# Kernel tuning notes

Measured on AMD Instinct MI355X. Metric: run time of the kernel, lower is better.

Reference implementation:

```python
import jax, jax.numpy as jnp
import numpy as np

N = 8192
IN_F = 512
OUT_F = 64
ALPHA = 0.2  # LeakyReLU negative slope
NEG_INF = -9e15


def setup_inputs() -> dict:
    key = jax.random.key(0)
    k1, k2, k3, k4 = jax.random.split(key, 4)
    inp = jax.random.normal(k1, (N, IN_F), dtype=jnp.float32)
    adj = jax.random.randint(k2, (N, N), 0, 2, dtype=jnp.int32)
    W = jax.random.normal(k3, (IN_F, OUT_F), dtype=jnp.float32) * (1.414 * (6.0 / (IN_F + OUT_F)) ** 0.5)
    a = jax.random.normal(k4, (2 * OUT_F, 1), dtype=jnp.float32) * (1.414 * (6.0 / (2 * OUT_F + 1)) ** 0.5)
    return {"input": inp, "adj": adj, "W": W, "a": a}


def reference(input, adj, W, a):
    h = input @ W                      # [N, F]
    F_ = h.shape[1]
    # e_ij = leakyrelu(a[:F].h_i + a[F:].h_j)  (equivalent to the concat form)
    f_src = h @ a[:F_, 0]              # [N]
    f_dst = h @ a[F_:, 0]              # [N]
    e = jax.nn.leaky_relu(f_src[:, None] + f_dst[None, :], negative_slope=ALPHA)  # [N, N]
    att = jnp.where(adj > 0, e, jnp.float32(NEG_INF))
    att = jax.nn.softmax(att, axis=1)  # dropout p is inert in eval mode
    h_prime = att @ h                  # [N, F]
    return jax.nn.elu(h_prime)         # concat=True
```

## Files before the change

### kernel.cpp

```cpp
#include <hip/hip_runtime.h>

#define N_NODES 8192
#define IN_F 512
#define OUT_F 64
#define LOG2E 1.4426950408889634f

typedef short bf16x8 __attribute__((ext_vector_type(8)));
typedef float f32x4 __attribute__((ext_vector_type(4)));

__global__ __launch_bounds__(256) void k_gemm(const float* __restrict__ input,
                                              const float* __restrict__ W,
                                              const float* __restrict__ a,
                                              unsigned short* __restrict__ hT,
                                              float* __restrict__ fsrcL,
                                              float* __restrict__ fdstL) {
  const int lane = threadIdx.x & 63;
  const int wv = threadIdx.x >> 6;
  const int r0 = blockIdx.x * 4;
  const int row = r0 + wv;
  const float* inrow = input + (size_t)row * IN_F;
  const int c = lane;
  float acc = 0.f;
  for (int k = 0; k < IN_F; k += 4) {
    float4 x = *(const float4*)(inrow + k);
    acc += x.x * W[(k + 0) * OUT_F + c];
    acc += x.y * W[(k + 1) * OUT_F + c];
    acc += x.z * W[(k + 2) * OUT_F + c];
    acc += x.w * W[(k + 3) * OUT_F + c];
  }
  float vs = acc * a[c];
  float vd = acc * a[OUT_F + c];
#pragma unroll
  for (int off = 32; off > 0; off >>= 1) {
    vs += __shfl_xor(vs, off, 64);
    vd += __shfl_xor(vd, off, 64);
  }
  if (lane == 0) {
    fsrcL[row] = vs * LOG2E;
    fdstL[row] = vd * LOG2E;
  }
  __shared__ float hs[4][64];
  hs[wv][c] = acc;
  __syncthreads();
  if (threadIdx.x < 64) {
    const int cc = threadIdx.x;
    unsigned u0 = __float_as_uint(hs[0][cc]) + 0x8000u;
    unsigned u1 = __float_as_uint(hs[1][cc]) + 0x8000u;
    unsigned u2 = __float_as_uint(hs[2][cc]) + 0x8000u;
    unsigned u3 = __float_as_uint(hs[3][cc]) + 0x8000u;
    uint2 pk;
    pk.x = __builtin_amdgcn_perm(u1, u0, 0x07060302u);
    pk.y = __builtin_amdgcn_perm(u3, u2, 0x07060302u);
    *(uint2*)(hT + (size_t)cc * N_NODES + r0) = pk;
  }
}

__global__ __launch_bounds__(256) void k_max(const float* __restrict__ fdstL,
                                             float* __restrict__ ML) {
  float m = -3.0e38f;
  for (int i = threadIdx.x; i < N_NODES; i += 256) m = fmaxf(m, fdstL[i]);
#pragma unroll
  for (int off = 32; off > 0; off >>= 1) m = fmaxf(m, __shfl_xor(m, off, 64));
  __shared__ float sm[4];
  if ((threadIdx.x & 63) == 0) sm[threadIdx.x >> 6] = m;
  __syncthreads();
  if (threadIdx.x == 0) ML[0] = fmaxf(fmaxf(sm[0], sm[1]), fmaxf(sm[2], sm[3]));
}

__global__ __launch_bounds__(512) void k_attn(const int* __restrict__ adj,
                                              const unsigned short* __restrict__ hT,
                                              const float* __restrict__ fsrcL,
                                              const float* __restrict__ fdstL,
                                              const float* __restrict__ MLp,
                                              float* __restrict__ out) {
  const int lane = threadIdx.x & 63;
  const int wv = threadIdx.x >> 6;
  const int i0 = blockIdx.x * 16;
  const int m = lane & 15;
  const int g = lane >> 4;

  const float MLv = MLp[0];
  const float fs = fsrcL[i0 + m];
  const float xm = fs + MLv;
  const float mL = fmaxf(xm, 0.2f * xm);

  f32x4 acc0{}, acc1{}, acc2{}, acc3{};
  float lpart = 0.f;

  const int* adjrow = adj + (size_t)(i0 + m) * N_NODES;
  const unsigned short* hT0 = hT + (size_t)m * N_NODES;

  const int jbeg = wv * (N_NODES / 8);
  for (int j0 = jbeg; j0 < jbeg + (N_NODES / 8); j0 += 64) {
#pragma unroll
    for (int s = 0; s < 2; s++) {
      const int jb = j0 + s * 32 + g * 8;
      int4 a0 = *(const int4*)(adjrow + jb);
      int4 a1 = *(const int4*)(adjrow + jb + 4);
      float4 d0 = *(const float4*)(fdstL + jb);
      float4 d1 = *(const float4*)(fdstL + jb + 4);
      bf16x8 b0 = *(const bf16x8*)(hT0 + jb);
      bf16x8 b1 = *(const bf16x8*)(hT0 + (size_t)16 * N_NODES + jb);
      bf16x8 b2 = *(const bf16x8*)(hT0 + (size_t)32 * N_NODES + jb);
      bf16x8 b3 = *(const bf16x8*)(hT0 + (size_t)48 * N_NODES + jb);

      const int av[8] = {a0.x, a0.y, a0.z, a0.w, a1.x, a1.y, a1.z, a1.w};
      const float dv[8] = {d0.x, d0.y, d0.z, d0.w, d1.x, d1.y, d1.z, d1.w};
      unsigned u[8];
#pragma unroll
      for (int t = 0; t < 8; t++) {
        float x = fs + dv[t];
        float y = fmaxf(x, 0.2f * x) - mL;
        float p = __builtin_amdgcn_exp2f(y);
        p = av[t] ? p : 0.0f;
        lpart += p;
        u[t] = __float_as_uint(p) + 0x8000u;
      }
      union { unsigned w[4]; bf16x8 v; } pc;
      pc.w[0] = __builtin_amdgcn_perm(u[1], u[0], 0x07060302u);
      pc.w[1] = __builtin_amdgcn_perm(u[3], u[2], 0x07060302u);
      pc.w[2] = __builtin_amdgcn_perm(u[5], u[4], 0x07060302u);
      pc.w[3] = __builtin_amdgcn_perm(u[7], u[6], 0x07060302u);

      acc0 = __builtin_amdgcn_mfma_f32_16x16x32_bf16(pc.v, b0, acc0, 0, 0, 0);
      acc1 = __builtin_amdgcn_mfma_f32_16x16x32_bf16(pc.v, b1, acc1, 0, 0, 0);
      acc2 = __builtin_amdgcn_mfma_f32_16x16x32_bf16(pc.v, b2, acc2, 0, 0, 0);
      acc3 = __builtin_amdgcn_mfma_f32_16x16x32_bf16(pc.v, b3, acc3, 0, 0, 0);
    }
  }

  lpart += __shfl_xor(lpart, 16, 64);
  lpart += __shfl_xor(lpart, 32, 64);

  __shared__ float accbuf[8][16][64];
  __shared__ float lbuf[8][16];
#pragma unroll
  for (int r = 0; r < 4; r++) {
    accbuf[wv][g * 4 + r][0 + m]  = acc0[r];
    accbuf[wv][g * 4 + r][16 + m] = acc1[r];
    accbuf[wv][g * 4 + r][32 + m] = acc2[r];
    accbuf[wv][g * 4 + r][48 + m] = acc3[r];
  }
  if (lane < 16) lbuf[wv][lane] = lpart;
  __syncthreads();

#pragma unroll
  for (int q = 0; q < 2; q++) {
    int idx = q * 512 + threadIdx.x;
    int r = idx >> 6, c = idx & 63;
    float ssum = 0.f, l = 0.f;
#pragma unroll
    for (int w = 0; w < 8; w++) {
      ssum += accbuf[w][r][c];
      l += lbuf[w][r];
    }
    float v = ssum / l;
    out[(size_t)(i0 + r) * OUT_F + c] =
        v > 0.f ? v : __builtin_amdgcn_exp2f(v * LOG2E) - 1.f;
  }
}

extern "C" void kernel_launch(void* const* d_in, const int* in_sizes, int n_in,
                              void* d_out, int out_size, void* d_ws, size_t ws_size,
                              hipStream_t stream) {
  const float* input = (const float*)d_in[0];
  const int* adj = (const int*)d_in[1];
  const float* W = (const float*)d_in[2];
  const float* a = (const float*)d_in[3];
  float* out = (float*)d_out;

  char* ws = (char*)d_ws;
  unsigned short* hT = (unsigned short*)ws;
  float* fsrcL = (float*)(ws + (1u << 20));
  float* fdstL = (float*)(ws + (1u << 20) + 32 * 1024);
  float* ML = (float*)(ws + (1u << 20) + 64 * 1024);

  k_gemm<<<N_NODES / 4, 256, 0, stream>>>(input, W, a, hT, fsrcL, fdstL);
  k_max<<<1, 256, 0, stream>>>(fdstL, ML);
  k_attn<<<N_NODES / 16, 512, 0, stream>>>(adj, hT, fsrcL, fdstL, ML, out);
}
```

Before: 511.4 us.

## Split attention over column blocks with merge kernel, register-tile input GEMM

The attention kernel now splits each 16-row block's neighbour range into four column chunks handled by separate 256-thread blocks. Each block writes partial numerators and denominators, and a new merge kernel sums them and applies the normalisation and ELU. The attention inner loop issues the loads for both 32-column halves up front to get more memory traffic in flight. The input projection kernel computes 8 rows per wave so each W load is reused across those rows, and it writes hT in wider 16-byte packets. The cost is an extra launch and a round trip of the partial sums through global memory.

```diff
diff --git a/kernel.cpp b/kernel.cpp
--- a/kernel.cpp
+++ b/kernel.cpp
@@ -4,6 +4,7 @@
 #define IN_F 512
 #define OUT_F 64
 #define LOG2E 1.4426950408889634f
+#define JSPLIT 4
 
 typedef short bf16x8 __attribute__((ext_vector_type(8)));
 typedef float f32x4 __attribute__((ext_vector_type(4)));
@@ -16,42 +17,53 @@
                                               float* __restrict__ fdstL) {
   const int lane = threadIdx.x & 63;
   const int wv = threadIdx.x >> 6;
-  const int r0 = blockIdx.x * 4;
-  const int row = r0 + wv;
-  const float* inrow = input + (size_t)row * IN_F;
+  const int r0 = blockIdx.x * 32;
+  const int rw = r0 + wv * 8;
   const int c = lane;
-  float acc = 0.f;
+  float acc[8] = {0.f, 0.f, 0.f, 0.f, 0.f, 0.f, 0.f, 0.f};
+  const float* Wc = W + c;
   for (int k = 0; k < IN_F; k += 4) {
-    float4 x = *(const float4*)(inrow + k);
-    acc += x.x * W[(k + 0) * OUT_F + c];
-    acc += x.y * W[(k + 1) * OUT_F + c];
-    acc += x.z * W[(k + 2) * OUT_F + c];
-    acc += x.w * W[(k + 3) * OUT_F + c];
-  }
-  float vs = acc * a[c];
-  float vd = acc * a[OUT_F + c];
-#pragma unroll
-  for (int off = 32; off > 0; off >>= 1) {
-    vs += __shfl_xor(vs, off, 64);
-    vd += __shfl_xor(vd, off, 64);
-  }
-  if (lane == 0) {
-    fsrcL[row] = vs * LOG2E;
-    fdstL[row] = vd * LOG2E;
-  }
-  __shared__ float hs[4][64];
-  hs[wv][c] = acc;
+    float w0 = Wc[(k + 0) * OUT_F];
+    float w1 = Wc[(k + 1) * OUT_F];
+    float w2 = Wc[(k + 2) * OUT_F];
+    float w3 = Wc[(k + 3) * OUT_F];
+#pragma unroll
+    for (int r = 0; r < 8; r++) {
+      float4 x = *(const float4*)(input + (size_t)(rw + r) * IN_F + k);
+      acc[r] += x.x * w0 + x.y * w1 + x.z * w2 + x.w * w3;
+    }
+  }
+#pragma unroll
+  for (int r = 0; r < 8; r++) {
+    float vs = acc[r] * a[c];
+    float vd = acc[r] * a[OUT_F + c];
+#pragma unroll
+    for (int off = 32; off > 0; off >>= 1) {
+      vs += __shfl_xor(vs, off, 64);
+      vd += __shfl_xor(vd, off, 64);
+    }
+    if (lane == 0) {
+      fsrcL[rw + r] = vs * LOG2E;
+      fdstL[rw + r] = vd * LOG2E;
+    }
+  }
+  __shared__ float hs[32][65];
+#pragma unroll
+  for (int r = 0; r < 8; r++) hs[wv * 8 + r][c] = acc[r];
   __syncthreads();
-  if (threadIdx.x < 64) {
-    const int cc = threadIdx.x;
-    unsigned u0 = __float_as_uint(hs[0][cc]) + 0x8000u;
-    unsigned u1 = __float_as_uint(hs[1][cc]) + 0x8000u;
-    unsigned u2 = __float_as_uint(hs[2][cc]) + 0x8000u;
-    unsigned u3 = __float_as_uint(hs[3][cc]) + 0x8000u;
-    uint2 pk;
-    pk.x = __builtin_amdgcn_perm(u1, u0, 0x07060302u);
-    pk.y = __builtin_amdgcn_perm(u3, u2, 0x07060302u);
-    *(uint2*)(hT + (size_t)cc * N_NODES + r0) = pk;
+  {
+    const int cc = threadIdx.x >> 2;
+    const int q = threadIdx.x & 3;
+    unsigned uu[8];
+#pragma unroll
+    for (int rr = 0; rr < 8; rr++)
+      uu[rr] = __float_as_uint(hs[q * 8 + rr][cc]) + 0x8000u;
+    uint4 pk;
+    pk.x = __builtin_amdgcn_perm(uu[1], uu[0], 0x07060302u);
+    pk.y = __builtin_amdgcn_perm(uu[3], uu[2], 0x07060302u);
+    pk.z = __builtin_amdgcn_perm(uu[5], uu[4], 0x07060302u);
+    pk.w = __builtin_amdgcn_perm(uu[7], uu[6], 0x07060302u);
+    *(uint4*)(hT + (size_t)cc * N_NODES + r0 + q * 8) = pk;
   }
 }
 
@@ -67,15 +79,18 @@
   if (threadIdx.x == 0) ML[0] = fmaxf(fmaxf(sm[0], sm[1]), fmaxf(sm[2], sm[3]));
 }
 
-__global__ __launch_bounds__(512) void k_attn(const int* __restrict__ adj,
+__global__ __launch_bounds__(256) void k_attn(const int* __restrict__ adj,
                                               const unsigned short* __restrict__ hT,
                                               const float* __restrict__ fsrcL,
                                               const float* __restrict__ fdstL,
                                               const float* __restrict__ MLp,
-                                              float* __restrict__ out) {
+                                              float* __restrict__ num,
+                                              float* __restrict__ den) {
   const int lane = threadIdx.x & 63;
   const int wv = threadIdx.x >> 6;
-  const int i0 = blockIdx.x * 16;
+  const int rb = blockIdx.x >> 2;
+  const int js = blockIdx.x & 3;
+  const int i0 = rb * 16;
   const int m = lane & 15;
   const int g = lane >> 4;
 
@@ -90,22 +105,29 @@
   const int* adjrow = adj + (size_t)(i0 + m) * N_NODES;
   const unsigned short* hT0 = hT + (size_t)m * N_NODES;
 
-  const int jbeg = wv * (N_NODES / 8);
-  for (int j0 = jbeg; j0 < jbeg + (N_NODES / 8); j0 += 64) {
-#pragma unroll
-    for (int s = 0; s < 2; s++) {
-      const int jb = j0 + s * 32 + g * 8;
-      int4 a0 = *(const int4*)(adjrow + jb);
-      int4 a1 = *(const int4*)(adjrow + jb + 4);
-      float4 d0 = *(const float4*)(fdstL + jb);
-      float4 d1 = *(const float4*)(fdstL + jb + 4);
-      bf16x8 b0 = *(const bf16x8*)(hT0 + jb);
-      bf16x8 b1 = *(const bf16x8*)(hT0 + (size_t)16 * N_NODES + jb);
-      bf16x8 b2 = *(const bf16x8*)(hT0 + (size_t)32 * N_NODES + jb);
-      bf16x8 b3 = *(const bf16x8*)(hT0 + (size_t)48 * N_NODES + jb);
-
-      const int av[8] = {a0.x, a0.y, a0.z, a0.w, a1.x, a1.y, a1.z, a1.w};
-      const float dv[8] = {d0.x, d0.y, d0.z, d0.w, d1.x, d1.y, d1.z, d1.w};
+  const int jbeg = js * (N_NODES / JSPLIT) + wv * 512;
+  for (int j0 = jbeg; j0 < jbeg + 512; j0 += 64) {
+    const int jb0 = j0 + g * 8;
+    const int jb1 = j0 + 32 + g * 8;
+    int4 a00 = *(const int4*)(adjrow + jb0);
+    int4 a01 = *(const int4*)(adjrow + jb0 + 4);
+    int4 a10 = *(const int4*)(adjrow + jb1);
+    int4 a11 = *(const int4*)(adjrow + jb1 + 4);
+    float4 d00 = *(const float4*)(fdstL + jb0);
+    float4 d01 = *(const float4*)(fdstL + jb0 + 4);
+    float4 d10 = *(const float4*)(fdstL + jb1);
+    float4 d11 = *(const float4*)(fdstL + jb1 + 4);
+    bf16x8 b00 = *(const bf16x8*)(hT0 + jb0);
+    bf16x8 b01 = *(const bf16x8*)(hT0 + (size_t)16 * N_NODES + jb0);
+    bf16x8 b02 = *(const bf16x8*)(hT0 + (size_t)32 * N_NODES + jb0);
+    bf16x8 b03 = *(const bf16x8*)(hT0 + (size_t)48 * N_NODES + jb0);
+    bf16x8 b10 = *(const bf16x8*)(hT0 + jb1);
+    bf16x8 b11 = *(const bf16x8*)(hT0 + (size_t)16 * N_NODES + jb1);
+    bf16x8 b12 = *(const bf16x8*)(hT0 + (size_t)32 * N_NODES + jb1);
+    bf16x8 b13 = *(const bf16x8*)(hT0 + (size_t)48 * N_NODES + jb1);
+    {
+      const int av[8] = {a00.x, a00.y, a00.z, a00.w, a01.x, a01.y, a01.z, a01.w};
+      const float dv[8] = {d00.x, d00.y, d00.z, d00.w, d01.x, d01.y, d01.z, d01.w};
       unsigned u[8];
 #pragma unroll
       for (int t = 0; t < 8; t++) {
@@ -121,19 +143,41 @@
       pc.w[1] = __builtin_amdgcn_perm(u[3], u[2], 0x07060302u);
       pc.w[2] = __builtin_amdgcn_perm(u[5], u[4], 0x07060302u);
       pc.w[3] = __builtin_amdgcn_perm(u[7], u[6], 0x07060302u);
-
-      acc0 = __builtin_amdgcn_mfma_f32_16x16x32_bf16(pc.v, b0, acc0, 0, 0, 0);
-      acc1 = __builtin_amdgcn_mfma_f32_16x16x32_bf16(pc.v, b1, acc1, 0, 0, 0);
-      acc2 = __builtin_amdgcn_mfma_f32_16x16x32_bf16(pc.v, b2, acc2, 0, 0, 0);
-      acc3 = __builtin_amdgcn_mfma_f32_16x16x32_bf16(pc.v, b3, acc3, 0, 0, 0);
+      acc0 = __builtin_amdgcn_mfma_f32_16x16x32_bf16(pc.v, b00, acc0, 0, 0, 0);
+      acc1 = __builtin_amdgcn_mfma_f32_16x16x32_bf16(pc.v, b01, acc1, 0, 0, 0);
+      acc2 = __builtin_amdgcn_mfma_f32_16x16x32_bf16(pc.v, b02, acc2, 0, 0, 0);
+      acc3 = __builtin_amdgcn_mfma_f32_16x16x32_bf16(pc.v, b03, acc3, 0, 0, 0);
+    }
+    {
+      const int av[8] = {a10.x, a10.y, a10.z, a10.w, a11.x, a11.y, a11.z, a11.w};
+      const float dv[8] = {d10.x, d10.y, d10.z, d10.w, d11.x, d11.y, d11.z, d11.w};
+      unsigned u[8];
+#pragma unroll
+      for (int t = 0; t < 8; t++) {
+        float x = fs + dv[t];
+        float y = fmaxf(x, 0.2f * x) - mL;
+        float p = __builtin_amdgcn_exp2f(y);
+        p = av[t] ? p : 0.0f;
+        lpart += p;
+        u[t] = __float_as_uint(p) + 0x8000u;
+      }
+      union { unsigned w[4]; bf16x8 v; } pc;
+      pc.w[0] = __builtin_amdgcn_perm(u[1], u[0], 0x07060302u);
+      pc.w[1] = __builtin_amdgcn_perm(u[3], u[2], 0x07060302u);
+      pc.w[2] = __builtin_amdgcn_perm(u[5], u[4], 0x07060302u);
+      pc.w[3] = __builtin_amdgcn_perm(u[7], u[6], 0x07060302u);
+      acc0 = __builtin_amdgcn_mfma_f32_16x16x32_bf16(pc.v, b10, acc0, 0, 0, 0);
+      acc1 = __builtin_amdgcn_mfma_f32_16x16x32_bf16(pc.v, b11, acc1, 0, 0, 0);
+      acc2 = __builtin_amdgcn_mfma_f32_16x16x32_bf16(pc.v, b12, acc2, 0, 0, 0);
+      acc3 = __builtin_amdgcn_mfma_f32_16x16x32_bf16(pc.v, b13, acc3, 0, 0, 0);
     }
   }
 
   lpart += __shfl_xor(lpart, 16, 64);
   lpart += __shfl_xor(lpart, 32, 64);
 
-  __shared__ float accbuf[8][16][64];
-  __shared__ float lbuf[8][16];
+  __shared__ float accbuf[4][16][64];
+  __shared__ float lbuf[4][16];
 #pragma unroll
   for (int r = 0; r < 4; r++) {
     accbuf[wv][g * 4 + r][0 + m]  = acc0[r];
@@ -145,19 +189,31 @@
   __syncthreads();
 
 #pragma unroll
-  for (int q = 0; q < 2; q++) {
-    int idx = q * 512 + threadIdx.x;
+  for (int q = 0; q < 4; q++) {
+    int idx = q * 256 + threadIdx.x;
     int r = idx >> 6, c = idx & 63;
-    float ssum = 0.f, l = 0.f;
-#pragma unroll
-    for (int w = 0; w < 8; w++) {
-      ssum += accbuf[w][r][c];
-      l += lbuf[w][r];
-    }
-    float v = ssum / l;
-    out[(size_t)(i0 + r) * OUT_F + c] =
-        v > 0.f ? v : __builtin_amdgcn_exp2f(v * LOG2E) - 1.f;
-  }
+    float ssum = accbuf[0][r][c] + accbuf[1][r][c] + accbuf[2][r][c] + accbuf[3][r][c];
+    num[((size_t)js * N_NODES + i0 + r) * OUT_F + c] = ssum;
+  }
+  if (threadIdx.x < 16) {
+    den[(size_t)js * N_NODES + i0 + threadIdx.x] =
+        lbuf[0][threadIdx.x] + lbuf[1][threadIdx.x] + lbuf[2][threadIdx.x] + lbuf[3][threadIdx.x];
+  }
+}
+
+__global__ __launch_bounds__(256) void k_merge(const float* __restrict__ num,
+                                               const float* __restrict__ den,
+                                               float* __restrict__ out) {
+  const int idx = blockIdx.x * 256 + threadIdx.x;
+  const int i = idx >> 6;
+  float s = 0.f, l = 0.f;
+#pragma unroll
+  for (int js = 0; js < JSPLIT; js++) {
+    s += num[((size_t)js * N_NODES) * OUT_F + idx];
+    l += den[(size_t)js * N_NODES + i];
+  }
+  float v = s / l;
+  out[idx] = v > 0.f ? v : __builtin_amdgcn_exp2f(v * LOG2E) - 1.f;
 }
 
 extern "C" void kernel_launch(void* const* d_in, const int* in_sizes, int n_in,
@@ -174,8 +230,11 @@
   float* fsrcL = (float*)(ws + (1u << 20));
   float* fdstL = (float*)(ws + (1u << 20) + 32 * 1024);
   float* ML = (float*)(ws + (1u << 20) + 64 * 1024);
-
-  k_gemm<<<N_NODES / 4, 256, 0, stream>>>(input, W, a, hT, fsrcL, fdstL);
+  float* num = (float*)(ws + (2u << 20));
+  float* den = (float*)(ws + (10u << 20));
+
+  k_gemm<<<N_NODES / 32, 256, 0, stream>>>(input, W, a, hT, fsrcL, fdstL);
   k_max<<<1, 256, 0, stream>>>(fdstL, ML);
-  k_attn<<<N_NODES / 16, 512, 0, stream>>>(adj, hT, fsrcL, fdstL, ML, out);
-}
+  k_attn<<<(N_NODES / 16) * JSPLIT, 256, 0, stream>>>(adj, hT, fsrcL, fdstL, ML, num, den);
+  k_merge<<<N_NODES * OUT_F / 256, 256, 0, stream>>>(num, den, out);
+}
```

Result: faster. 452.5 us (-11.5%).
